# Kernel tuning notes

Measured on AMD Instinct MI355X. Metric: run time of the kernel, lower is better.

The kernel has to match this reference:

```python
import jax, jax.numpy as jnp
import numpy as np

B, N, DIM = 8, 1024, 768
HEADS, DHEAD = 12, 64
INNER = HEADS * DHEAD  # 768
ALPHA = 0.25
SCALE = DHEAD ** -0.5
EPS = 1e-5


def setup_inputs() -> dict:
    key = jax.random.key(0)
    ks = jax.random.split(key, 7)
    x = jax.random.normal(ks[0], (B, N, DIM), dtype=jnp.float32)
    h = jax.random.normal(ks[1], (B, HEADS, N, N), dtype=jnp.float32)
    gamma = jnp.ones((DIM,), dtype=jnp.float32)
    beta = jnp.zeros((DIM,), dtype=jnp.float32)
    w_qkv = jax.random.normal(ks[2], (DIM, 3 * INNER), dtype=jnp.float32) * (DIM ** -0.5)
    w_out = jax.random.normal(ks[3], (INNER, DIM), dtype=jnp.float32) * (INNER ** -0.5)
    b_out = jnp.zeros((DIM,), dtype=jnp.float32)
    return {"x": x, "h": h, "gamma": gamma, "beta": beta,
            "w_qkv": w_qkv, "w_out": w_out, "b_out": b_out}


def reference(x, h, gamma, beta, w_qkv, w_out, b_out):
    # LayerNorm over last dim
    mu = jnp.mean(x, axis=-1, keepdims=True)
    var = jnp.mean(jnp.square(x - mu), axis=-1, keepdims=True)
    xn = (x - mu) * jax.lax.rsqrt(var + EPS) * gamma + beta
    # fused QKV projection (no bias)
    qkv = xn @ w_qkv                                     # (b, n, 3*inner)
    q, k, v = jnp.split(qkv, 3, axis=-1)
    split_heads = lambda t: t.reshape(B, N, HEADS, DHEAD).transpose(0, 2, 1, 3)  # b h n d
    q, k, v = split_heads(q), split_heads(k), split_heads(v)
    raw = jnp.einsum('bhid,bhjd->bhij', q, k) * SCALE    # (b, h, n, n)
    blended = ALPHA * raw + (1.0 - ALPHA) * h
    attn = jax.nn.softmax(blended, axis=-1)              # dropout p=0 -> identity
    out = jnp.einsum('bhij,bhjd->bhid', attn, v)         # (b, h, n, d)
    out = out.transpose(0, 2, 1, 3).reshape(B, N, INNER)
    out = out @ w_out + b_out
    return (out, blended)
```

## Files before the change

kernel.cpp:

```cpp
#include <hip/hip_runtime.h>
#include <hip/hip_bf16.h>
#include <stdint.h>

#define NB 8
#define NSEQ 1024
#define DIMM 768
#define NHEADS 12
#define DH 64
#define NQKV 2304
#define ALPHA_ 0.25f
#define SCALE_ 0.125f
#define EPS_ 1e-5f

typedef __bf16 bf16;
typedef bf16 bf16x8 __attribute__((ext_vector_type(8)));
typedef bf16 bf16x4 __attribute__((ext_vector_type(4)));
typedef float f32x4 __attribute__((ext_vector_type(4)));

#define MFMA16(a, b, c) __builtin_amdgcn_mfma_f32_16x16x32_bf16((a), (b), (c), 0, 0, 0)

static __device__ __forceinline__ void load_lds16(const void* gsrc, void* ldst) {
  __builtin_amdgcn_global_load_lds(
      (__attribute__((address_space(1))) void*)gsrc,
      (__attribute__((address_space(3))) void*)ldst, 16, 0, 0);
}

#define BAR_LGKM()                                             \
  do {                                                         \
    __builtin_amdgcn_sched_barrier(0);                         \
    asm volatile("s_waitcnt lgkmcnt(0)" ::: "memory");         \
    __builtin_amdgcn_s_barrier();                              \
    __builtin_amdgcn_sched_barrier(0);                         \
  } while (0)

static __device__ __forceinline__ int swz(int row, int cb) {
  return cb ^ ((((row & 7) ^ ((cb >> 7) & 7)) << 4));
}

__global__ __launch_bounds__(256) void ln_kernel(
    const float* __restrict__ x, const float* __restrict__ gamma,
    const float* __restrict__ beta, bf16* __restrict__ xn) {
  const int row = blockIdx.x * 4 + (threadIdx.x >> 6);
  const int lane = threadIdx.x & 63;
  const float* xr = x + (size_t)row * DIMM;
  float4 v[3];
  float s = 0.f, s2 = 0.f;
#pragma unroll
  for (int c = 0; c < 3; ++c) {
    v[c] = *reinterpret_cast<const float4*>(xr + c * 256 + lane * 4);
    s += v[c].x + v[c].y + v[c].z + v[c].w;
    s2 += v[c].x * v[c].x + v[c].y * v[c].y + v[c].z * v[c].z + v[c].w * v[c].w;
  }
#pragma unroll
  for (int m = 1; m < 64; m <<= 1) {
    s += __shfl_xor(s, m);
    s2 += __shfl_xor(s2, m);
  }
  const float mu = s * (1.f / DIMM);
  const float rstd = rsqrtf(s2 * (1.f / DIMM) - mu * mu + EPS_);
#pragma unroll
  for (int c = 0; c < 3; ++c) {
    const float4 g4 = *reinterpret_cast<const float4*>(gamma + c * 256 + lane * 4);
    const float4 b4 = *reinterpret_cast<const float4*>(beta + c * 256 + lane * 4);
    bf16x4 o;
    o[0] = (bf16)((v[c].x - mu) * rstd * g4.x + b4.x);
    o[1] = (bf16)((v[c].y - mu) * rstd * g4.y + b4.y);
    o[2] = (bf16)((v[c].z - mu) * rstd * g4.z + b4.z);
    o[3] = (bf16)((v[c].w - mu) * rstd * g4.w + b4.w);
    *reinterpret_cast<bf16x4*>(xn + (size_t)row * DIMM + c * 256 + lane * 4) = o;
  }
}

__global__ __launch_bounds__(256) void tcast_kernel(
    const float* __restrict__ in, bf16* __restrict__ out, int R, int C) {
  __shared__ float tile[32][33];
  const int tx = threadIdx.x & 31, ty = threadIdx.x >> 5;
  const int c0 = blockIdx.x * 32, r0 = blockIdx.y * 32;
#pragma unroll
  for (int i = ty; i < 32; i += 8)
    tile[i][tx] = in[(size_t)(r0 + i) * C + c0 + tx];
  __syncthreads();
#pragma unroll
  for (int i = ty; i < 32; i += 8)
    out[(size_t)(c0 + i) * R + r0 + tx] = (bf16)tile[tx][i];
}

__global__ __launch_bounds__(256) void qkv_gemm(
    const bf16* __restrict__ xn, const bf16* __restrict__ wT,
    bf16* __restrict__ qb, bf16* __restrict__ kb, bf16* __restrict__ vt) {
  __shared__ __align__(16) bf16 As[128 * 32];
  __shared__ __align__(16) bf16 Bs[64 * 32];
  const int tid = threadIdx.x;
  const int wv = tid >> 6, l = tid & 63;
  const int l16 = l & 15, q4 = l >> 4;
  const int c0 = blockIdx.x * 64, row0 = blockIdx.y * 128;
  const int sr = tid >> 2, skk = (tid & 3) * 8;
  f32x4 acc0[4], acc1[4];
#pragma unroll
  for (int c = 0; c < 4; ++c) {
    acc0[c] = f32x4{0.f, 0.f, 0.f, 0.f};
    acc1[c] = f32x4{0.f, 0.f, 0.f, 0.f};
  }
  for (int k0 = 0; k0 < DIMM; k0 += 32) {
    __syncthreads();
    load_lds16(xn + (size_t)(row0 + sr) * DIMM + k0 + skk, As + tid * 8);
    load_lds16(xn + (size_t)(row0 + 64 + sr) * DIMM + k0 + skk, As + 2048 + tid * 8);
    load_lds16(wT + (size_t)(c0 + sr) * DIMM + k0 + skk, Bs + tid * 8);
    __syncthreads();
    const bf16x8 a0 = *reinterpret_cast<const bf16x8*>(&As[(wv * 32 + l16) * 32 + q4 * 8]);
    const bf16x8 a1 = *reinterpret_cast<const bf16x8*>(&As[(wv * 32 + 16 + l16) * 32 + q4 * 8]);
#pragma unroll
    for (int c = 0; c < 4; ++c) {
      const bf16x8 bb = *reinterpret_cast<const bf16x8*>(&Bs[(c * 16 + l16) * 32 + q4 * 8]);
      acc0[c] = MFMA16(a0, bb, acc0[c]);
      acc1[c] = MFMA16(a1, bb, acc1[c]);
    }
  }
  const int sect = c0 / DIMM;
  const int head = (c0 % DIMM) >> 6;
#pragma unroll
  for (int c = 0; c < 4; ++c) {
    const int dd = c * 16 + l16;
#pragma unroll
    for (int r = 0; r < 4; ++r) {
#pragma unroll
      for (int rsub = 0; rsub < 2; ++rsub) {
        const int gm = row0 + wv * 32 + rsub * 16 + q4 * 4 + r;
        const int b = gm >> 10, n = gm & 1023;
        const size_t bhh = (size_t)b * NHEADS + head;
        const float av = rsub ? acc1[c][r] : acc0[c][r];
        const bf16 val = (bf16)av;
        if (sect == 0)      qb[(bhh * NSEQ + n) * DH + dd] = val;
        else if (sect == 1) kb[(bhh * NSEQ + n) * DH + dd] = val;
        else                vt[(bhh * DH + dd) * NSEQ + n] = val;
      }
    }
  }
}

__global__ __launch_bounds__(256, 4) void attn_kernel(
    const bf16* __restrict__ qb, const bf16* __restrict__ kb,
    const bf16* __restrict__ vt, const float* __restrict__ h,
    float* __restrict__ blended, bf16* __restrict__ attn_out) {
  __shared__ __align__(16) char S_lds[16 * 2176];
  __shared__ float lred[16];

  const int tid = threadIdx.x;
  const int wv = tid >> 6, l = tid & 63;
  const int l16 = l & 15, q4 = l >> 4;
  const int i0 = blockIdx.x * 16;
  const int bh = blockIdx.y;
  const int jb = wv * 256;

  const float* hbase = h + ((size_t)bh << 20);
  float* bbase = blended + ((size_t)bh << 20);

  bf16x8 qT[2];
#pragma unroll
  for (int w2 = 0; w2 < 2; ++w2)
    qT[w2] = *reinterpret_cast<const bf16x8*>(
        qb + ((size_t)bh * NSEQ + i0 + l16) * DH + w2 * 32 + q4 * 8);

  float4 hv0[4], hv1[4];
#pragma unroll
  for (int t = 0; t < 4; ++t) {
    hv0[t] = *reinterpret_cast<const float4*>(
        hbase + (size_t)(i0 + wv * 4 + 0) * NSEQ + t * 256 + l * 4);
    hv1[t] = *reinterpret_cast<const float4*>(
        hbase + (size_t)(i0 + wv * 4 + 1) * NSEQ + t * 256 + l * 4);
  }

  const bf16* kq = kb + ((size_t)bh * NSEQ + jb + l16) * DH + q4 * 8;
  char* srow_w = S_lds + l16 * 2176;
#pragma unroll
  for (int st = 0; st < 4; ++st) {
    f32x4 s[4];
#pragma unroll
    for (int js = 0; js < 4; ++js) s[js] = f32x4{0.f, 0.f, 0.f, 0.f};
#pragma unroll
    for (int js = 0; js < 4; ++js) {
#pragma unroll
      for (int w2 = 0; w2 < 2; ++w2) {
        const bf16x8 kf = *reinterpret_cast<const bf16x8*>(
            kq + (size_t)(st * 64 + js * 16) * DH + w2 * 32);
        s[js] = MFMA16(kf, qT[w2], s[js]);
      }
    }
#pragma unroll
    for (int js = 0; js < 4; ++js) {
      bf16x4 pk;
#pragma unroll
      for (int r = 0; r < 4; ++r) pk[r] = (bf16)(s[js][r] * (ALPHA_ * SCALE_));
      const int cb = (jb + st * 64 + js * 16 + q4 * 4) * 2;
      *reinterpret_cast<bf16x4*>(srow_w + swz(l16, cb)) = pk;
    }
  }

  float4 hv2[4], hv3[4];
#pragma unroll
  for (int t = 0; t < 4; ++t) {
    hv2[t] = *reinterpret_cast<const float4*>(
        hbase + (size_t)(i0 + wv * 4 + 2) * NSEQ + t * 256 + l * 4);
    hv3[t] = *reinterpret_cast<const float4*>(
        hbase + (size_t)(i0 + wv * 4 + 3) * NSEQ + t * 256 + l * 4);
  }

  BAR_LGKM();

  auto ROW = [&](int rr, float4* hv) {
    const int row = wv * 4 + rr;
    char* srow = S_lds + row * 2176;
    bf16x4 sv[4];
#pragma unroll
    for (int t = 0; t < 4; ++t)
      sv[t] = *reinterpret_cast<const bf16x4*>(srow + swz(row, t * 512 + l * 8));
    float4 bl[4];
    float tm = -1e30f;
#pragma unroll
    for (int t = 0; t < 4; ++t) {
      bl[t].x = fmaf(0.75f, hv[t].x, (float)sv[t][0]);
      bl[t].y = fmaf(0.75f, hv[t].y, (float)sv[t][1]);
      bl[t].z = fmaf(0.75f, hv[t].z, (float)sv[t][2]);
      bl[t].w = fmaf(0.75f, hv[t].w, (float)sv[t][3]);
      *reinterpret_cast<float4*>(
          bbase + (size_t)(i0 + row) * NSEQ + t * 256 + l * 4) = bl[t];
      tm = fmaxf(tm, fmaxf(fmaxf(bl[t].x, bl[t].y), fmaxf(bl[t].z, bl[t].w)));
    }
#pragma unroll
    for (int mm = 1; mm < 64; mm <<= 1) tm = fmaxf(tm, __shfl_xor(tm, mm));
    float rs = 0.f;
#pragma unroll
    for (int t = 0; t < 4; ++t) {
      bf16x4 pk;
      const float p0 = __expf(bl[t].x - tm); rs += p0; pk[0] = (bf16)p0;
      const float p1 = __expf(bl[t].y - tm); rs += p1; pk[1] = (bf16)p1;
      const float p2 = __expf(bl[t].z - tm); rs += p2; pk[2] = (bf16)p2;
      const float p3 = __expf(bl[t].w - tm); rs += p3; pk[3] = (bf16)p3;
      *reinterpret_cast<bf16x4*>(srow + swz(row, t * 512 + l * 8)) = pk;
    }
#pragma unroll
    for (int mm = 1; mm < 64; mm <<= 1) rs += __shfl_xor(rs, mm);
    if (l == 0) lred[row] = rs;
  };
  ROW(0, hv0);
  ROW(1, hv1);
  ROW(2, hv2);
  ROW(3, hv3);

  BAR_LGKM();

  const bf16* vq = vt + ((size_t)bh * DH + wv * 16 + l16) * NSEQ + q4 * 8;
  char* prow = S_lds + l16 * 2176;
  f32x4 a0 = f32x4{0.f, 0.f, 0.f, 0.f}, a1 = a0, a2 = a0, a3 = a0;
#pragma unroll
  for (int ks = 0; ks < 32; ks += 4) {
    const bf16x8 pa0 = *reinterpret_cast<const bf16x8*>(prow + swz(l16, (ks + 0) * 64 + q4 * 16));
    const bf16x8 vf0 = *reinterpret_cast<const bf16x8*>(vq + (ks + 0) * 32);
    a0 = MFMA16(pa0, vf0, a0);
    const bf16x8 pa1 = *reinterpret_cast<const bf16x8*>(prow + swz(l16, (ks + 1) * 64 + q4 * 16));
    const bf16x8 vf1 = *reinterpret_cast<const bf16x8*>(vq + (ks + 1) * 32);
    a1 = MFMA16(pa1, vf1, a1);
    const bf16x8 pa2 = *reinterpret_cast<const bf16x8*>(prow + swz(l16, (ks + 2) * 64 + q4 * 16));
    const bf16x8 vf2 = *reinterpret_cast<const bf16x8*>(vq + (ks + 2) * 32);
    a2 = MFMA16(pa2, vf2, a2);
    const bf16x8 pa3 = *reinterpret_cast<const bf16x8*>(prow + swz(l16, (ks + 3) * 64 + q4 * 16));
    const bf16x8 vf3 = *reinterpret_cast<const bf16x8*>(vq + (ks + 3) * 32);
    a3 = MFMA16(pa3, vf3, a3);
  }
  const f32x4 af = (a0 + a1) + (a2 + a3);
  const int b = bh / NHEADS, head = bh % NHEADS;
#pragma unroll
  for (int r = 0; r < 4; ++r) {
    const int q = q4 * 4 + r;
    attn_out[((size_t)b * NSEQ + i0 + q) * DIMM + head * DH + wv * 16 + l16] =
        (bf16)(af[r] / lred[q]);
  }
}

__global__ __launch_bounds__(256) void oproj_gemm(
    const bf16* __restrict__ ain, const bf16* __restrict__ wT,
    const float* __restrict__ bias, float* __restrict__ out) {
  __shared__ __align__(16) bf16 As[128 * 32];
  __shared__ __align__(16) bf16 Bs[64 * 32];
  const int tid = threadIdx.x;
  const int wv = tid >> 6, l = tid & 63;
  const int l16 = l & 15, q4 = l >> 4;
  const int c0 = blockIdx.x * 64, row0 = blockIdx.y * 128;
  const int sr = tid >> 2, skk = (tid & 3) * 8;
  f32x4 acc0[4], acc1[4];
#pragma unroll
  for (int c = 0; c < 4; ++c) {
    acc0[c] = f32x4{0.f, 0.f, 0.f, 0.f};
    acc1[c] = f32x4{0.f, 0.f, 0.f, 0.f};
  }
  for (int k0 = 0; k0 < DIMM; k0 += 32) {
    __syncthreads();
    load_lds16(ain + (size_t)(row0 + sr) * DIMM + k0 + skk, As + tid * 8);
    load_lds16(ain + (size_t)(row0 + 64 + sr) * DIMM + k0 + skk, As + 2048 + tid * 8);
    load_lds16(wT + (size_t)(c0 + sr) * DIMM + k0 + skk, Bs + tid * 8);
    __syncthreads();
    const bf16x8 a0 = *reinterpret_cast<const bf16x8*>(&As[(wv * 32 + l16) * 32 + q4 * 8]);
    const bf16x8 a1 = *reinterpret_cast<const bf16x8*>(&As[(wv * 32 + 16 + l16) * 32 + q4 * 8]);
#pragma unroll
    for (int c = 0; c < 4; ++c) {
      const bf16x8 bb = *reinterpret_cast<const bf16x8*>(&Bs[(c * 16 + l16) * 32 + q4 * 8]);
      acc0[c] = MFMA16(a0, bb, acc0[c]);
      acc1[c] = MFMA16(a1, bb, acc1[c]);
    }
  }
#pragma unroll
  for (int c = 0; c < 4; ++c) {
    const int gc = c0 + c * 16 + l16;
    const float bv = bias[gc];
#pragma unroll
    for (int r = 0; r < 4; ++r) {
      out[(size_t)(row0 + wv * 32 + q4 * 4 + r) * DIMM + gc] = acc0[c][r] + bv;
      out[(size_t)(row0 + wv * 32 + 16 + q4 * 4 + r) * DIMM + gc] = acc1[c][r] + bv;
    }
  }
}

extern "C" void kernel_launch(void* const* d_in, const int* in_sizes, int n_in,
                              void* d_out, int out_size, void* d_ws, size_t ws_size,
                              hipStream_t stream) {
  const float* x = (const float*)d_in[0];
  const float* h = (const float*)d_in[1];
  const float* gamma = (const float*)d_in[2];
  const float* beta = (const float*)d_in[3];
  const float* w_qkv = (const float*)d_in[4];
  const float* w_out = (const float*)d_in[5];
  const float* b_out = (const float*)d_in[6];
  float* out = (float*)d_out;
  float* blended = out + (size_t)NB * NSEQ * DIMM;

  char* ws = (char*)d_ws;
  bf16* xn = (bf16*)(ws);
  bf16* qb = (bf16*)(ws + 12582912);
  bf16* kb = (bf16*)(ws + 25165824);
  bf16* vt = (bf16*)(ws + 37748736);
  bf16* wqkvT = (bf16*)(ws + 50331648);
  bf16* woutT = (bf16*)(ws + 53870592);

  hipLaunchKernelGGL(ln_kernel, dim3(2048), dim3(256), 0, stream, x, gamma, beta, xn);
  hipLaunchKernelGGL(tcast_kernel, dim3(72, 24), dim3(256), 0, stream, w_qkv, wqkvT, DIMM, NQKV);
  hipLaunchKernelGGL(tcast_kernel, dim3(24, 24), dim3(256), 0, stream, w_out, woutT, DIMM, DIMM);
  hipLaunchKernelGGL(qkv_gemm, dim3(36, 64), dim3(256), 0, stream, xn, wqkvT, qb, kb, vt);
  hipLaunchKernelGGL(attn_kernel, dim3(64, 96), dim3(256), 0, stream, qb, kb, vt, h, blended, xn);
  hipLaunchKernelGGL(oproj_gemm, dim3(12, 64), dim3(256), 0, stream, xn, woutT, b_out, out);
}
```

Measured before the change: 387.0 us.

## Split attention rows into two key chunks with online softmax to halve LDS

The attention kernel now processes the 1024 keys in two 512-wide chunks, using an online-softmax running max and sum with rescaling of the PV accumulators between chunks. This halves the LDS score buffer and drops the register-held h prefetch, so launch bounds can target 8 blocks per SM instead of 4. The h reads and blended writes also become nontemporal loads and stores. In exchange the kernel adds extra barriers, exp rescaling work, and loses the early prefetch of h that overlapped the QK MFMAs.

```diff
diff --git a/kernel.cpp b/kernel.cpp
--- a/kernel.cpp
+++ b/kernel.cpp
@@ -138,22 +138,24 @@
   }
 }
 
-__global__ __launch_bounds__(256, 4) void attn_kernel(
+__global__ __launch_bounds__(256, 8) void attn_kernel(
     const bf16* __restrict__ qb, const bf16* __restrict__ kb,
     const bf16* __restrict__ vt, const float* __restrict__ h,
     float* __restrict__ blended, bf16* __restrict__ attn_out) {
-  __shared__ __align__(16) char S_lds[16 * 2176];
-  __shared__ float lred[16];
+  __shared__ __align__(16) char S_lds[16 * 1152];
+  __shared__ __align__(16) float scl[16];
+  __shared__ __align__(16) float lred[16];
 
   const int tid = threadIdx.x;
   const int wv = tid >> 6, l = tid & 63;
   const int l16 = l & 15, q4 = l >> 4;
   const int i0 = blockIdx.x * 16;
   const int bh = blockIdx.y;
-  const int jb = wv * 256;
 
   const float* hbase = h + ((size_t)bh << 20);
   float* bbase = blended + ((size_t)bh << 20);
+  const bf16* kbase = kb + (size_t)bh * NSEQ * DH;
+  const bf16* vbase = vt + (size_t)bh * DH * NSEQ;
 
   bf16x8 qT[2];
 #pragma unroll
@@ -161,119 +163,119 @@
     qT[w2] = *reinterpret_cast<const bf16x8*>(
         qb + ((size_t)bh * NSEQ + i0 + l16) * DH + w2 * 32 + q4 * 8);
 
-  float4 hv0[4], hv1[4];
-#pragma unroll
-  for (int t = 0; t < 4; ++t) {
-    hv0[t] = *reinterpret_cast<const float4*>(
-        hbase + (size_t)(i0 + wv * 4 + 0) * NSEQ + t * 256 + l * 4);
-    hv1[t] = *reinterpret_cast<const float4*>(
-        hbase + (size_t)(i0 + wv * 4 + 1) * NSEQ + t * 256 + l * 4);
-  }
-
-  const bf16* kq = kb + ((size_t)bh * NSEQ + jb + l16) * DH + q4 * 8;
-  char* srow_w = S_lds + l16 * 2176;
-#pragma unroll
-  for (int st = 0; st < 4; ++st) {
-    f32x4 s[4];
-#pragma unroll
-    for (int js = 0; js < 4; ++js) s[js] = f32x4{0.f, 0.f, 0.f, 0.f};
-#pragma unroll
-    for (int js = 0; js < 4; ++js) {
-#pragma unroll
-      for (int w2 = 0; w2 < 2; ++w2) {
-        const bf16x8 kf = *reinterpret_cast<const bf16x8*>(
-            kq + (size_t)(st * 64 + js * 16) * DH + w2 * 32);
-        s[js] = MFMA16(kf, qT[w2], s[js]);
-      }
-    }
-#pragma unroll
-    for (int js = 0; js < 4; ++js) {
-      bf16x4 pk;
-#pragma unroll
-      for (int r = 0; r < 4; ++r) pk[r] = (bf16)(s[js][r] * (ALPHA_ * SCALE_));
-      const int cb = (jb + st * 64 + js * 16 + q4 * 4) * 2;
-      *reinterpret_cast<bf16x4*>(srow_w + swz(l16, cb)) = pk;
-    }
-  }
-
-  float4 hv2[4], hv3[4];
-#pragma unroll
-  for (int t = 0; t < 4; ++t) {
-    hv2[t] = *reinterpret_cast<const float4*>(
-        hbase + (size_t)(i0 + wv * 4 + 2) * NSEQ + t * 256 + l * 4);
-    hv3[t] = *reinterpret_cast<const float4*>(
-        hbase + (size_t)(i0 + wv * 4 + 3) * NSEQ + t * 256 + l * 4);
-  }
-
-  BAR_LGKM();
-
-  auto ROW = [&](int rr, float4* hv) {
-    const int row = wv * 4 + rr;
-    char* srow = S_lds + row * 2176;
-    bf16x4 sv[4];
-#pragma unroll
-    for (int t = 0; t < 4; ++t)
-      sv[t] = *reinterpret_cast<const bf16x4*>(srow + swz(row, t * 512 + l * 8));
-    float4 bl[4];
-    float tm = -1e30f;
-#pragma unroll
-    for (int t = 0; t < 4; ++t) {
-      bl[t].x = fmaf(0.75f, hv[t].x, (float)sv[t][0]);
-      bl[t].y = fmaf(0.75f, hv[t].y, (float)sv[t][1]);
-      bl[t].z = fmaf(0.75f, hv[t].z, (float)sv[t][2]);
-      bl[t].w = fmaf(0.75f, hv[t].w, (float)sv[t][3]);
-      *reinterpret_cast<float4*>(
-          bbase + (size_t)(i0 + row) * NSEQ + t * 256 + l * 4) = bl[t];
-      tm = fmaxf(tm, fmaxf(fmaxf(bl[t].x, bl[t].y), fmaxf(bl[t].z, bl[t].w)));
-    }
-#pragma unroll
-    for (int mm = 1; mm < 64; mm <<= 1) tm = fmaxf(tm, __shfl_xor(tm, mm));
-    float rs = 0.f;
-#pragma unroll
-    for (int t = 0; t < 4; ++t) {
-      bf16x4 pk;
-      const float p0 = __expf(bl[t].x - tm); rs += p0; pk[0] = (bf16)p0;
-      const float p1 = __expf(bl[t].y - tm); rs += p1; pk[1] = (bf16)p1;
-      const float p2 = __expf(bl[t].z - tm); rs += p2; pk[2] = (bf16)p2;
-      const float p3 = __expf(bl[t].w - tm); rs += p3; pk[3] = (bf16)p3;
-      *reinterpret_cast<bf16x4*>(srow + swz(row, t * 512 + l * 8)) = pk;
-    }
-#pragma unroll
-    for (int mm = 1; mm < 64; mm <<= 1) rs += __shfl_xor(rs, mm);
-    if (l == 0) lred[row] = rs;
-  };
-  ROW(0, hv0);
-  ROW(1, hv1);
-  ROW(2, hv2);
-  ROW(3, hv3);
-
-  BAR_LGKM();
-
-  const bf16* vq = vt + ((size_t)bh * DH + wv * 16 + l16) * NSEQ + q4 * 8;
-  char* prow = S_lds + l16 * 2176;
-  f32x4 a0 = f32x4{0.f, 0.f, 0.f, 0.f}, a1 = a0, a2 = a0, a3 = a0;
-#pragma unroll
-  for (int ks = 0; ks < 32; ks += 4) {
-    const bf16x8 pa0 = *reinterpret_cast<const bf16x8*>(prow + swz(l16, (ks + 0) * 64 + q4 * 16));
-    const bf16x8 vf0 = *reinterpret_cast<const bf16x8*>(vq + (ks + 0) * 32);
-    a0 = MFMA16(pa0, vf0, a0);
-    const bf16x8 pa1 = *reinterpret_cast<const bf16x8*>(prow + swz(l16, (ks + 1) * 64 + q4 * 16));
-    const bf16x8 vf1 = *reinterpret_cast<const bf16x8*>(vq + (ks + 1) * 32);
-    a1 = MFMA16(pa1, vf1, a1);
-    const bf16x8 pa2 = *reinterpret_cast<const bf16x8*>(prow + swz(l16, (ks + 2) * 64 + q4 * 16));
-    const bf16x8 vf2 = *reinterpret_cast<const bf16x8*>(vq + (ks + 2) * 32);
-    a2 = MFMA16(pa2, vf2, a2);
-    const bf16x8 pa3 = *reinterpret_cast<const bf16x8*>(prow + swz(l16, (ks + 3) * 64 + q4 * 16));
-    const bf16x8 vf3 = *reinterpret_cast<const bf16x8*>(vq + (ks + 3) * 32);
-    a3 = MFMA16(pa3, vf3, a3);
-  }
-  const f32x4 af = (a0 + a1) + (a2 + a3);
+  f32x4 acc[4];
+#pragma unroll
+  for (int kk = 0; kk < 4; ++kk) acc[kk] = f32x4{0.f, 0.f, 0.f, 0.f};
+  float m_run[4], l_run[4];
+#pragma unroll
+  for (int r = 0; r < 4; ++r) { m_run[r] = -1e30f; l_run[r] = 0.f; }
+
+#pragma unroll
+  for (int c = 0; c < 2; ++c) {
+    {
+      const bf16* kq = kbase + (size_t)(c * 512 + wv * 128 + l16) * DH + q4 * 8;
+      char* srow_w = S_lds + l16 * 1152;
+#pragma unroll
+      for (int st = 0; st < 2; ++st) {
+        f32x4 s[4];
+#pragma unroll
+        for (int js = 0; js < 4; ++js) s[js] = f32x4{0.f, 0.f, 0.f, 0.f};
+#pragma unroll
+        for (int js = 0; js < 4; ++js) {
+#pragma unroll
+          for (int w2 = 0; w2 < 2; ++w2) {
+            const bf16x8 kf = *reinterpret_cast<const bf16x8*>(
+                kq + (size_t)(st * 64 + js * 16) * DH + w2 * 32);
+            s[js] = MFMA16(kf, qT[w2], s[js]);
+          }
+        }
+#pragma unroll
+        for (int js = 0; js < 4; ++js) {
+          bf16x4 pk;
+#pragma unroll
+          for (int r = 0; r < 4; ++r) pk[r] = (bf16)(s[js][r] * (ALPHA_ * SCALE_));
+          const int cb = (wv * 256 + st * 128 + js * 32 + q4 * 8);
+          *reinterpret_cast<bf16x4*>(srow_w + swz(l16, cb)) = pk;
+        }
+      }
+    }
+    BAR_LGKM();
+
+#pragma unroll
+    for (int rr = 0; rr < 4; ++rr) {
+      const int row = wv * 4 + rr;
+      char* srow = S_lds + row * 1152;
+      const bf16x8 sv = *reinterpret_cast<const bf16x8*>(srow + swz(row, l * 16));
+      const float* hp = hbase + (size_t)(i0 + row) * NSEQ + c * 512 + l * 8;
+      const f32x4 h0 = __builtin_nontemporal_load(reinterpret_cast<const f32x4*>(hp));
+      const f32x4 h1 = __builtin_nontemporal_load(reinterpret_cast<const f32x4*>(hp + 4));
+      float bl[8];
+#pragma unroll
+      for (int t = 0; t < 4; ++t) bl[t] = fmaf(0.75f, h0[t], (float)sv[t]);
+#pragma unroll
+      for (int t = 0; t < 4; ++t) bl[4 + t] = fmaf(0.75f, h1[t], (float)sv[4 + t]);
+      float* bp = bbase + (size_t)(i0 + row) * NSEQ + c * 512 + l * 8;
+      f32x4 b0, b1;
+#pragma unroll
+      for (int t = 0; t < 4; ++t) { b0[t] = bl[t]; b1[t] = bl[4 + t]; }
+      __builtin_nontemporal_store(b0, reinterpret_cast<f32x4*>(bp));
+      __builtin_nontemporal_store(b1, reinterpret_cast<f32x4*>(bp + 4));
+      float tm = bl[0];
+#pragma unroll
+      for (int t = 1; t < 8; ++t) tm = fmaxf(tm, bl[t]);
+#pragma unroll
+      for (int mm = 1; mm < 64; mm <<= 1) tm = fmaxf(tm, __shfl_xor(tm, mm));
+      const float mnew = fmaxf(m_run[rr], tm);
+      const float sc = __expf(m_run[rr] - mnew);
+      m_run[rr] = mnew;
+      float rs = 0.f;
+      bf16x8 pk;
+#pragma unroll
+      for (int t = 0; t < 8; ++t) {
+        const float p = __expf(bl[t] - mnew);
+        rs += p;
+        pk[t] = (bf16)p;
+      }
+      *reinterpret_cast<bf16x8*>(srow + swz(row, l * 16)) = pk;
+#pragma unroll
+      for (int mm = 1; mm < 64; mm <<= 1) rs += __shfl_xor(rs, mm);
+      l_run[rr] = l_run[rr] * sc + rs;
+      if (l == 0) {
+        scl[row] = sc;
+        if (c == 1) lred[row] = l_run[rr];
+      }
+    }
+    BAR_LGKM();
+
+    {
+      const f32x4 sclv = *reinterpret_cast<const f32x4*>(&scl[q4 * 4]);
+      const bf16* vq = vbase + (size_t)(wv * 16 + l16) * NSEQ + c * 512 + q4 * 8;
+      char* prow = S_lds + l16 * 1152;
+#pragma unroll
+      for (int kk = 0; kk < 4; ++kk) acc[kk] *= sclv;
+#pragma unroll
+      for (int kk = 0; kk < 4; ++kk) {
+#pragma unroll
+        for (int ki = 0; ki < 4; ++ki) {
+          const int ks = kk * 4 + ki;
+          const bf16x8 pa = *reinterpret_cast<const bf16x8*>(
+              prow + swz(l16, ks * 64 + q4 * 16));
+          const bf16x8 vf = *reinterpret_cast<const bf16x8*>(vq + ks * 32);
+          acc[kk] = MFMA16(pa, vf, acc[kk]);
+        }
+      }
+    }
+    if (c == 0) BAR_LGKM();
+  }
+
+  const f32x4 lv = *reinterpret_cast<const f32x4*>(&lred[q4 * 4]);
+  const f32x4 af = (acc[0] + acc[1]) + (acc[2] + acc[3]);
   const int b = bh / NHEADS, head = bh % NHEADS;
 #pragma unroll
   for (int r = 0; r < 4; ++r) {
     const int q = q4 * 4 + r;
     attn_out[((size_t)b * NSEQ + i0 + q) * DIMM + head * DH + wv * 16 + l16] =
-        (bf16)(af[r] / lred[q]);
+        (bf16)(af[r] / lv[r]);
   }
 }
 
```

Result: slower. 538.7 us (+39.2%).
